# Optimization experiments

Measured on AMD Instinct MI355X. Metric: run time of the kernel, lower is better.

## Reference

```python
import jax, jax.numpy as jnp
import numpy as np

N, E = 50000, 800000
ND, ED, H, L = 128, 32, 128, 4


def _mlp2(x, w1, b1, w2, b2):
    return jax.nn.relu(x @ w1 + b1) @ w2 + b2


def _layer_norm(x, g, b, eps=1e-5):
    m = jnp.mean(x, axis=-1, keepdims=True)
    v = jnp.var(x, axis=-1, keepdims=True)
    return (x - m) * jax.lax.rsqrt(v + eps) * g + b


def setup_inputs() -> dict:
    key = jax.random.key(0)
    ks = iter(jax.random.split(key, 40))
    r = lambda *s: jax.random.normal(next(ks), s, jnp.float32) * 0.05
    return dict(
        x=r(N, ND),
        edge_attr=r(E, ED),
        h_prev=r(N, H),
        enc_w1=r(ND, H), enc_b1=jnp.zeros((H,), jnp.float32),
        enc_w2=r(H, H), enc_b2=jnp.zeros((H,), jnp.float32),
        et_w1=r(L, 2 * H + ED, H), et_b1=jnp.zeros((L, H), jnp.float32),
        et_w2=r(L, H, H), et_b2=jnp.zeros((L, H), jnp.float32),
        msg_w1=r(L, H, H), msg_b1=jnp.zeros((L, H), jnp.float32),
        msg_w2=r(L, H, H), msg_b2=jnp.zeros((L, H), jnp.float32),
        upd_w1=r(L, 2 * H, H), upd_b1=jnp.zeros((L, H), jnp.float32),
        upd_w2=r(L, H, H), upd_b2=jnp.zeros((L, H), jnp.float32),
        ln_g=jnp.ones((H,), jnp.float32), ln_b=jnp.zeros((H,), jnp.float32),
        gru_wih=r(3 * H, H), gru_whh=r(3 * H, H),
        gru_bih=jnp.zeros((3 * H,), jnp.float32),
        gru_bhh=jnp.zeros((3 * H,), jnp.float32),
        edge_index=jax.random.randint(next(ks), (2, E), 0, N, jnp.int32),
    )


def reference(x, edge_attr, h_prev,
              enc_w1, enc_b1, enc_w2, enc_b2,
              et_w1, et_b1, et_w2, et_b2,
              msg_w1, msg_b1, msg_w2, msg_b2,
              upd_w1, upd_b1, upd_w2, upd_b2,
              ln_g, ln_b,
              gru_wih, gru_whh, gru_bih, gru_bhh,
              edge_index):
    src, dst = edge_index[0], edge_index[1]  # PyG: x_j = x[src], x_i = x[dst]
    n_nodes = x.shape[0]
    h = _mlp2(x, enc_w1, enc_b1, enc_w2, enc_b2)  # [N, H]
    for l in range(et_w1.shape[0]):
        x_i = h[dst]                                  # [E, H] gather (target)
        x_j = h[src]                                  # [E, H] gather (source)
        e_in = jnp.concatenate([x_i, x_j, edge_attr], axis=-1)  # [E, 2H+ED]
        e_emb = _mlp2(e_in, et_w1[l], et_b1[l], et_w2[l], et_b2[l])
        msg = _mlp2(e_emb, msg_w1[l], msg_b1[l], msg_w2[l], msg_b2[l])
        aggr = jax.ops.segment_sum(msg, dst, num_segments=n_nodes)  # [N, H]
        h_new = _mlp2(jnp.concatenate([h, aggr], axis=-1),
                      upd_w1[l], upd_b1[l], upd_w2[l], upd_b2[l])
        h = _layer_norm(h + h_new, ln_g, ln_b)
    # GRUCell(input=h, hidden=h_prev), torch semantics
    gi = h @ gru_wih.T + gru_bih          # [N, 3H]
    gh = h_prev @ gru_whh.T + gru_bhh     # [N, 3H]
    i_r, i_z, i_n = jnp.split(gi, 3, axis=-1)
    h_r, h_z, h_n = jnp.split(gh, 3, axis=-1)
    r = jax.nn.sigmoid(i_r + h_r)
    z = jax.nn.sigmoid(i_z + h_z)
    n = jnp.tanh(i_n + r * h_n)
    return (1.0 - z) * n + z * h_prev
```

## Files before the change

### kernel.cpp

```cpp
#include <hip/hip_runtime.h>
#include <hip/hip_bf16.h>
#include <cstdint>

#define NN 50000
#define NE 800000

typedef _Float16 f16;
typedef f16 f16x8 __attribute__((ext_vector_type(8)));
typedef f16 f16x4 __attribute__((ext_vector_type(4)));
typedef float f32x4 __attribute__((ext_vector_type(4)));

#define TB_STR 136

__global__ void hist_kernel(const int* __restrict__ edst, int* __restrict__ deg) {
  int e = blockIdx.x * 256 + threadIdx.x;
  if (e < NE) atomicAdd(&deg[edst[e]], 1);
}

__global__ void scan_kernel(const int* __restrict__ deg, int* __restrict__ offs, int n) {
  __shared__ int tmp[256];
  __shared__ int carry;
  const int tid = threadIdx.x;
  if (tid == 0) carry = 0;
  __syncthreads();
  for (int base = 0; base < n; base += 1024) {
    int v[4]; int s = 0;
#pragma unroll
    for (int j = 0; j < 4; ++j) {
      int idx = base + tid * 4 + j;
      v[j] = (idx < n) ? deg[idx] : 0;
      s += v[j];
    }
    tmp[tid] = s;
    __syncthreads();
    for (int ofs = 1; ofs < 256; ofs <<= 1) {
      int t = (tid >= ofs) ? tmp[tid - ofs] : 0;
      __syncthreads();
      tmp[tid] += t;
      __syncthreads();
    }
    int excl = carry + tmp[tid] - s;
#pragma unroll
    for (int j = 0; j < 4; ++j) {
      int idx = base + tid * 4 + j;
      if (idx < n) offs[idx] = excl;
      excl += v[j];
    }
    __syncthreads();
    if (tid == 255) carry += tmp[255];
    __syncthreads();
  }
  if (tid == 0) offs[n] = carry;
}

__global__ void copy_cursor_kernel(const int* __restrict__ offs, int* __restrict__ cursor) {
  int i = blockIdx.x * 256 + threadIdx.x;
  if (i < NN) cursor[i] = offs[i];
}

__global__ void fill_kernel(const int* __restrict__ edst, int* __restrict__ cursor,
                            int* __restrict__ eord) {
  int e = blockIdx.x * 256 + threadIdx.x;
  if (e < NE) {
    int p = atomicAdd(&cursor[edst[e]], 1);
    eord[p] = e;
  }
}

__global__ void permute_kernel(const int* __restrict__ eord,
                               const int* __restrict__ esrc,
                               const int* __restrict__ edst,
                               const float* __restrict__ ea,
                               int* __restrict__ dstp, int* __restrict__ esp,
                               f16* __restrict__ ea16p) {
  int i = blockIdx.x * 256 + threadIdx.x;
  if (i >= NE) return;
  int e = eord[i];
  dstp[i] = edst[e];
  esp[i] = esrc[e];
  const float* sp = ea + (size_t)e * 32;
  f16* dp = ea16p + (size_t)i * 32;
#pragma unroll
  for (int j = 0; j < 4; ++j) {
    float4 u0 = *(const float4*)(sp + j * 8), u1 = *(const float4*)(sp + j * 8 + 4);
    f16x8 v = {(f16)u0.x, (f16)u0.y, (f16)u0.z, (f16)u0.w,
               (f16)u1.x, (f16)u1.y, (f16)u1.z, (f16)u1.w};
    *(f16x8*)(dp + j * 8) = v;
  }
}

__global__ void pack_w_kernel(const float* __restrict__ et_w1,
                              const float* __restrict__ et_w2,
                              const float* __restrict__ msg_w1,
                              const float* __restrict__ msg_w2,
                              f16* __restrict__ wpack) {
  int idx = blockIdx.x * 256 + threadIdx.x;
  if (idx >= 4 * 86016) return;
  int l = idx / 86016;
  int rem = idx - l * 86016;
  int unit = rem >> 9;
  int e = rem & 511;
  int ln = e >> 3, i = e & 7;
  const float* src;
  int ul;
  if (unit < 72)       { src = et_w1  + (size_t)l * 288 * 128; ul = unit; }
  else if (unit < 104) { src = et_w2  + (size_t)l * 128 * 128; ul = unit - 72; }
  else if (unit < 136) { src = msg_w1 + (size_t)l * 128 * 128; ul = unit - 104; }
  else                 { src = msg_w2 + (size_t)l * 128 * 128; ul = unit - 136; }
  int kc = ul >> 3, ct = ul & 7;
  int k = kc * 32 + (ln >> 4) * 8 + i;
  int col = ct * 16 + (ln & 15);
  wpack[idx] = (f16)src[k * 128 + col];
}

__global__ void pack_upd_kernel(const float* __restrict__ upd_w1,
                                const float* __restrict__ upd_w2,
                                f16* __restrict__ wpu) {
  int idx = blockIdx.x * 256 + threadIdx.x;
  if (idx >= 4 * 96 * 512) return;
  int l = idx / (96 * 512);
  int rem = idx - l * (96 * 512);
  int unit = rem >> 9, e = rem & 511, ln = e >> 3, i = e & 7;
  const float* src;
  int ul;
  if (unit < 64) { src = upd_w1 + (size_t)l * 256 * 128; ul = unit; }
  else           { src = upd_w2 + (size_t)l * 128 * 128; ul = unit - 64; }
  int kc = ul >> 3, ct = ul & 7;
  int k = kc * 32 + (ln >> 4) * 8 + i;
  int col = ct * 16 + (ln & 15);
  wpu[idx] = (f16)src[k * 128 + col];
}

__global__ void pack_gru_kernel(const float* __restrict__ wih,
                                const float* __restrict__ whh,
                                const float* __restrict__ bih,
                                const float* __restrict__ bhh,
                                f16* __restrict__ wg, float* __restrict__ brz) {
  int idx = blockIdx.x * 256 + threadIdx.x;
  if (idx < 256) brz[idx] = bih[idx] + bhh[idx];
  if (idx >= 192 * 512) return;
  int unit = idx >> 9, e = idx & 511, ln = e >> 3, i = e & 7;
  int krow = (ln >> 4) * 8 + i;
  int cl16 = ln & 15;
  f16 val;
  if (unit < 128) {
    int kc = unit >> 4, ctg = unit & 15;
    int k = kc * 32 + krow;
    int col = ctg * 16 + cl16;
    float w = (k < 128) ? wih[col * 128 + k] : whh[col * 128 + (k - 128)];
    val = (f16)w;
  } else if (unit < 160) {
    int ul = unit - 128;
    int k = (ul >> 3) * 32 + krow;
    int col = (ul & 7) * 16 + cl16;
    val = (f16)wih[(256 + col) * 128 + k];
  } else {
    int ul = unit - 160;
    int k = (ul >> 3) * 32 + krow;
    int col = (ul & 7) * 16 + cl16;
    val = (f16)whh[(256 + col) * 128 + k];
  }
  wg[idx] = val;
}

__global__ void pack_enc_kernel(const float* __restrict__ w1,
                                const float* __restrict__ w2,
                                f16* __restrict__ wpenc) {
  int idx = blockIdx.x * 256 + threadIdx.x;
  if (idx >= 64 * 512) return;
  int unit = idx >> 9, e = idx & 511, ln = e >> 3, i = e & 7;
  const float* src = (unit < 32) ? w1 : w2;
  int ul = unit & 31;
  int k = (ul >> 3) * 32 + (ln >> 4) * 8 + i;
  int col = (ul & 7) * 16 + (ln & 15);
  wpenc[idx] = (f16)src[k * 128 + col];
}

__global__ void cvt_x_kernel(const float* __restrict__ x, f16* __restrict__ x16) {
  int idx = blockIdx.x * 256 + threadIdx.x;
  if (idx >= NN * 16) return;
  const float* sp = x + (size_t)idx * 8;
  float4 u0 = *(const float4*)sp, u1 = *(const float4*)(sp + 4);
  f16x8 v = {(f16)u0.x, (f16)u0.y, (f16)u0.z, (f16)u0.w,
             (f16)u1.x, (f16)u1.y, (f16)u1.z, (f16)u1.w};
  *(f16x8*)(x16 + (size_t)idx * 8) = v;
}

#define EDGE_ACC_INIT(BIAS)                                                    \
  _Pragma("unroll") for (int ct = 0; ct < 4; ++ct) {                           \
    float bv_ = (BIAS)[wc * 64 + ct * 16 + cl];                                \
    acc[0][ct] = (f32x4){bv_, bv_, bv_, bv_};                                  \
    acc[1][ct] = acc[0][ct];                                                   \
  }

#define EDGE_MFMA_KC(A0, A1, UNIT)                                             \
  _Pragma("unroll") for (int ct = 0; ct < 4; ++ct) {                           \
    f16x8 b_ = *(const f16x8*)&wp[(size_t)(((UNIT) + wc * 4 + ct) * 64 + lane) * 8]; \
    acc[0][ct] = __builtin_amdgcn_mfma_f32_16x16x32_f16(A0, b_, acc[0][ct], 0, 0, 0); \
    acc[1][ct] = __builtin_amdgcn_mfma_f32_16x16x32_f16(A1, b_, acc[1][ct], 0, 0, 0); \
  }

#define EDGE_GEMM_LDS(APTR, UNIT0, BIAS)                                       \
  {                                                                            \
    EDGE_ACC_INIT(BIAS);                                                       \
    _Pragma("unroll") for (int kc = 0; kc < 4; ++kc) {                         \
      f16x8 a0_ = *(const f16x8*)&(APTR)[(wr * 32 + cl) * TB_STR + kc * 32 + kh * 8]; \
      f16x8 a1_ = *(const f16x8*)&(APTR)[(wr * 32 + 16 + cl) * TB_STR + kc * 32 + kh * 8]; \
      EDGE_MFMA_KC(a0_, a1_, (UNIT0) + kc * 8);                                \
    }                                                                          \
  }

#define EDGE_STORE(DST, RELU)                                                  \
  _Pragma("unroll") for (int rt = 0; rt < 2; ++rt)                             \
    _Pragma("unroll") for (int ct = 0; ct < 4; ++ct)                           \
      _Pragma("unroll") for (int i = 0; i < 4; ++i) {                          \
        float v_ = acc[rt][ct][i];                                             \
        if (RELU) v_ = fmaxf(v_, 0.f);                                         \
        (DST)[(wr * 32 + rt * 16 + kh * 4 + i) * TB_STR + wc * 64 + ct * 16 + cl] = (f16)v_; \
      }

__global__ __launch_bounds__(256, 6)
void edge_mfma_kernel(const f16* __restrict__ h16, const f16* __restrict__ ea16p,
                      const int* __restrict__ esp, const int* __restrict__ dstp,
                      const f16* __restrict__ wp,
                      const float* __restrict__ b1, const float* __restrict__ b2,
                      const float* __restrict__ b3, const float* __restrict__ b4,
                      float* __restrict__ aggrf) {
  __shared__ f16 buf[64 * TB_STR];
  __shared__ int eidx[128];
  const int tid = threadIdx.x;
  const int lane = tid & 63;
  const int wv = tid >> 6;
  const int wr = wv >> 1, wc = wv & 1;
  const int cl = lane & 15;
  const int kh = lane >> 4;
  const int e0 = blockIdx.x * 64;
  if (tid < 64) eidx[tid] = dstp[e0 + tid];
  else if (tid < 128) eidx[tid] = esp[e0 + tid - 64];
  __syncthreads();

  const int r0 = wr * 32 + cl, r1 = r0 + 16;
  const f16* pd0 = h16 + (size_t)eidx[r0] * 128 + kh * 8;
  const f16* pd1 = h16 + (size_t)eidx[r1] * 128 + kh * 8;
  const f16* ps0 = h16 + (size_t)eidx[64 + r0] * 128 + kh * 8;
  const f16* ps1 = h16 + (size_t)eidx[64 + r1] * 128 + kh * 8;
  const f16* pe0 = ea16p + (size_t)(e0 + r0) * 32 + kh * 8;
  const f16* pe1 = ea16p + (size_t)(e0 + r1) * 32 + kh * 8;

  f32x4 acc[2][4];
  EDGE_ACC_INIT(b1);
#pragma unroll
  for (int kc = 0; kc < 4; ++kc) {
    f16x8 a0_ = *(const f16x8*)(pd0 + kc * 32);
    f16x8 a1_ = *(const f16x8*)(pd1 + kc * 32);
    EDGE_MFMA_KC(a0_, a1_, kc * 8);
  }
#pragma unroll
  for (int kc = 4; kc < 8; ++kc) {
    f16x8 a0_ = *(const f16x8*)(ps0 + (kc - 4) * 32);
    f16x8 a1_ = *(const f16x8*)(ps1 + (kc - 4) * 32);
    EDGE_MFMA_KC(a0_, a1_, kc * 8);
  }
  {
    f16x8 a0_ = *(const f16x8*)pe0;
    f16x8 a1_ = *(const f16x8*)pe1;
    EDGE_MFMA_KC(a0_, a1_, 64);
  }
  EDGE_STORE(buf, 1);
  __syncthreads();
  EDGE_GEMM_LDS(buf, 72, b2);
  __syncthreads();
  EDGE_STORE(buf, 0);
  __syncthreads();
  EDGE_GEMM_LDS(buf, 104, b3);
  __syncthreads();
  EDGE_STORE(buf, 1);
  __syncthreads();
  EDGE_GEMM_LDS(buf, 136, b4);
  __syncthreads();
  EDGE_STORE(buf, 0);
  __syncthreads();
  {
    const int c = tid & 127;
    const int rbeg = (tid >> 7) * 32;
    float sum = 0.f;
    int cur = eidx[rbeg];
    bool openL = true;
    for (int r = rbeg; r < rbeg + 32; ++r) {
      sum += (float)buf[r * TB_STR + c];
      bool last = (r == rbeg + 31);
      int nxt = last ? -1 : eidx[r + 1];
      if (last || nxt != cur) {
        float* ap = aggrf + (size_t)cur * 128 + c;
        if (openL || last) unsafeAtomicAdd(ap, sum);
        else *ap = sum;
        sum = 0.f; cur = nxt; openL = false;
      }
    }
  }
}

__global__ __launch_bounds__(256, 4)
void encoder_mfma_kernel(const f16* __restrict__ x16, const f16* __restrict__ wp,
                         const float* __restrict__ b1, const float* __restrict__ b2,
                         f16* __restrict__ h16out) {
  __shared__ f16 buf[64 * TB_STR];
  const int tid = threadIdx.x;
  const int lane = tid & 63;
  const int wv = tid >> 6;
  const int wr = wv >> 1, wc = wv & 1;
  const int cl = lane & 15;
  const int kh = lane >> 4;
  const int r0 = blockIdx.x * 64;
  const int gr0 = min(r0 + wr * 32 + cl, NN - 1);
  const int gr1 = min(r0 + wr * 32 + 16 + cl, NN - 1);
  const f16* px0 = x16 + (size_t)gr0 * 128 + kh * 8;
  const f16* px1 = x16 + (size_t)gr1 * 128 + kh * 8;
  f32x4 acc[2][4];
  EDGE_ACC_INIT(b1);
#pragma unroll
  for (int kc = 0; kc < 4; ++kc) {
    f16x8 a0_ = *(const f16x8*)(px0 + kc * 32);
    f16x8 a1_ = *(const f16x8*)(px1 + kc * 32);
    EDGE_MFMA_KC(a0_, a1_, kc * 8);
  }
  EDGE_STORE(buf, 1);
  __syncthreads();
  EDGE_GEMM_LDS(buf, 32, b2);
  __syncthreads();
  EDGE_STORE(buf, 0);
  __syncthreads();
#pragma unroll
  for (int it = 0; it < 4; ++it) {
    int f = tid + it * 256;
    int row = f >> 4, c8 = f & 15;
    int grow = r0 + row;
    if (grow < NN) {
      f16x8 v = *(const f16x8*)&buf[row * TB_STR + c8 * 8];
      *(f16x8*)(h16out + (size_t)grow * 128 + c8 * 8) = v;
    }
  }
}

__global__ __launch_bounds__(256, 2)
void gru_mfma_kernel(const f16* __restrict__ h16, const float* __restrict__ hprev,
                     const f16* __restrict__ wg, const float* __restrict__ brz,
                     const float* __restrict__ bih, const float* __restrict__ bhh,
                     float* __restrict__ out) {
  __shared__ f16 ac[64 * 264];
  __shared__ f16 rz[64 * 264];
  const int tid = threadIdx.x;
  const int lane = tid & 63;
  const int wv = tid >> 6;
  const int wr = wv >> 1, wc = wv & 1;
  const int cl = lane & 15;
  const int kh = lane >> 4;
  const int r0 = blockIdx.x * 64;
#pragma unroll
  for (int it = 0; it < 8; ++it) {
    int f = tid + it * 256;
    int row = f >> 5, c8 = f & 31;
    int grow = r0 + row;
    f16x8 v = {};
    if (grow < NN) {
      if (c8 < 16) {
        v = *(const f16x8*)(h16 + (size_t)grow * 128 + c8 * 8);
      } else {
        const float* sp = hprev + (size_t)grow * 128 + (c8 - 16) * 8;
        float4 u0 = *(const float4*)sp, u1 = *(const float4*)(sp + 4);
        v = (f16x8){(f16)u0.x, (f16)u0.y, (f16)u0.z, (f16)u0.w,
                    (f16)u1.x, (f16)u1.y, (f16)u1.z, (f16)u1.w};
      }
    }
    *(f16x8*)&ac[row * 264 + c8 * 8] = v;
  }
  __syncthreads();
  {
    f32x4 az[4][4];
#pragma unroll
    for (int ct = 0; ct < 4; ++ct) {
      float bv = brz[wv * 64 + ct * 16 + cl];
#pragma unroll
      for (int rt = 0; rt < 4; ++rt) az[rt][ct] = (f32x4){bv, bv, bv, bv};
    }
#pragma unroll
    for (int kc = 0; kc < 8; ++kc) {
      f16x8 a_[4];
#pragma unroll
      for (int rt = 0; rt < 4; ++rt)
        a_[rt] = *(const f16x8*)&ac[(rt * 16 + cl) * 264 + kc * 32 + kh * 8];
#pragma unroll
      for (int ct = 0; ct < 4; ++ct) {
        f16x8 b_ = *(const f16x8*)&wg[(size_t)((kc * 16 + wv * 4 + ct) * 64 + lane) * 8];
#pragma unroll
        for (int rt = 0; rt < 4; ++rt)
          az[rt][ct] = __builtin_amdgcn_mfma_f32_16x16x32_f16(a_[rt], b_, az[rt][ct], 0, 0, 0);
      }
    }
#pragma unroll
    for (int rt = 0; rt < 4; ++rt)
#pragma unroll
      for (int ct = 0; ct < 4; ++ct)
#pragma unroll
        for (int i = 0; i < 4; ++i) {
          float sg = 1.f / (1.f + __expf(-az[rt][ct][i]));
          rz[(rt * 16 + kh * 4 + i) * 264 + wv * 64 + ct * 16 + cl] = (f16)sg;
        }
  }
  __syncthreads();
  f32x4 ai_[2][4], ah_[2][4];
#pragma unroll
  for (int ct = 0; ct < 4; ++ct) {
    float bi = bih[256 + wc * 64 + ct * 16 + cl];
    float bh = bhh[256 + wc * 64 + ct * 16 + cl];
    ai_[0][ct] = (f32x4){bi, bi, bi, bi}; ai_[1][ct] = ai_[0][ct];
    ah_[0][ct] = (f32x4){bh, bh, bh, bh}; ah_[1][ct] = ah_[0][ct];
  }
#pragma unroll
  for (int kc = 0; kc < 4; ++kc) {
    f16x8 a0 = *(const f16x8*)&ac[(wr * 32 + cl) * 264 + kc * 32 + kh * 8];
    f16x8 a1 = *(const f16x8*)&ac[(wr * 32 + 16 + cl) * 264 + kc * 32 + kh * 8];
    f16x8 p0 = *(const f16x8*)&ac[(wr * 32 + cl) * 264 + 128 + kc * 32 + kh * 8];
    f16x8 p1 = *(const f16x8*)&ac[(wr * 32 + 16 + cl) * 264 + 128 + kc * 32 + kh * 8];
#pragma unroll
    for (int ct = 0; ct < 4; ++ct) {
      f16x8 bi_ = *(const f16x8*)&wg[(size_t)(((128 + kc * 8 + wc * 4 + ct)) * 64 + lane) * 8];
      f16x8 bh_ = *(const f16x8*)&wg[(size_t)(((160 + kc * 8 + wc * 4 + ct)) * 64 + lane) * 8];
      ai_[0][ct] = __builtin_amdgcn_mfma_f32_16x16x32_f16(a0, bi_, ai_[0][ct], 0, 0, 0);
      ai_[1][ct] = __builtin_amdgcn_mfma_f32_16x16x32_f16(a1, bi_, ai_[1][ct], 0, 0, 0);
      ah_[0][ct] = __builtin_amdgcn_mfma_f32_16x16x32_f16(p0, bh_, ah_[0][ct], 0, 0, 0);
      ah_[1][ct] = __builtin_amdgcn_mfma_f32_16x16x32_f16(p1, bh_, ah_[1][ct], 0, 0, 0);
    }
  }
#pragma unroll
  for (int rt = 0; rt < 2; ++rt)
#pragma unroll
    for (int ct = 0; ct < 4; ++ct)
#pragma unroll
      for (int i = 0; i < 4; ++i) {
        int row = wr * 32 + rt * 16 + kh * 4 + i;
        int col = wc * 64 + ct * 16 + cl;
        int grow = r0 + row;
        if (grow < NN) {
          float r_ = (float)rz[row * 264 + col];
          float z_ = (float)rz[row * 264 + 128 + col];
          float n_ = tanhf(ai_[rt][ct][i] + r_ * ah_[rt][ct][i]);
          float hpv = (float)ac[row * 264 + 128 + col];
          out[(size_t)grow * 128 + col] = (1.f - z_) * n_ + z_ * hpv;
        }
      }
}

#define MFMA_T(APTR, ASTR, ASWZ, NKC, UNIT0, BIAS)                             \
  {                                                                            \
    _Pragma("unroll") for (int nt = 0; nt < 2; ++nt) {                         \
      f32x4 bv_ = *(const f32x4*)((BIAS) + wv * 32 + nt * 16 + kh * 4);        \
      _Pragma("unroll") for (int et = 0; et < 4; ++et) acc[nt][et] = bv_;      \
    }                                                                          \
    _Pragma("unroll 2") for (int kc = 0; kc < (NKC); ++kc) {                   \
      f16x8 wfr_[2];                                                           \
      _Pragma("unroll") for (int nt = 0; nt < 2; ++nt)                         \
        wfr_[nt] = *(const f16x8*)&wp[(size_t)(((UNIT0) + kc * 8 + wv * 2 + nt) * 64 + lane) * 8]; \
      _Pragma("unroll") for (int et = 0; et < 4; ++et) {                       \
        int r_ = et * 16 + cl;                                                 \
        int idx_ = r_ * (ASTR) + kc * 32 + kh * 8;                             \
        if (ASWZ) idx_ ^= ((r_ & 7) << 3);                                     \
        f16x8 efr_ = *(const f16x8*)&(APTR)[idx_];                             \
        _Pragma("unroll") for (int nt = 0; nt < 2; ++nt)                       \
          acc[nt][et] = __builtin_amdgcn_mfma_f32_16x16x32_f16(wfr_[nt], efr_, acc[nt][et], 0, 0, 0); \
      }                                                                        \
    }                                                                          \
  }

#define STORE_T(DPTR, RELU)                                                    \
  _Pragma("unroll") for (int nt = 0; nt < 2; ++nt)                             \
    _Pragma("unroll") for (int et = 0; et < 4; ++et) {                         \
      float v0_ = acc[nt][et][0], v1_ = acc[nt][et][1],                        \
            v2_ = acc[nt][et][2], v3_ = acc[nt][et][3];                        \
      if (RELU) { v0_ = fmaxf(v0_, 0.f); v1_ = fmaxf(v1_, 0.f);                \
                  v2_ = fmaxf(v2_, 0.f); v3_ = fmaxf(v3_, 0.f); }              \
      int r_ = et * 16 + cl;                                                   \
      int idx_ = (r_ * 128 + wv * 32 + nt * 16 + kh * 4) ^ ((r_ & 7) << 3);    \
      *(f16x4*)&(DPTR)[idx_] = (f16x4){(f16)v0_, (f16)v1_, (f16)v2_, (f16)v3_};\
    }

__global__ __launch_bounds__(256, 2)
void update_mfma_kernel(const f16* __restrict__ h16, const float* __restrict__ aggr,
                        const f16* __restrict__ wp,
                        const float* __restrict__ b1, const float* __restrict__ b2,
                        const float* __restrict__ lng, const float* __restrict__ lnb,
                        f16* __restrict__ h16out) {
  __shared__ f16 ua[64 * 264];
  __shared__ f16 tb[64 * 128];
  __shared__ f16 emb[64 * 128];
  const int tid = threadIdx.x;
  const int lane = tid & 63;
  const int wv = tid >> 6;
  const int cl = lane & 15;
  const int kh = lane >> 4;
  const int r0 = blockIdx.x * 64;
#pragma unroll
  for (int it = 0; it < 8; ++it) {
    int f = tid + it * 256;
    int row = f >> 5, c8 = f & 31;
    int grow = r0 + row;
    f16x8 v = {};
    if (grow < NN) {
      if (c8 < 16) {
        v = *(const f16x8*)(h16 + (size_t)grow * 128 + c8 * 8);
      } else {
        const float* sp = aggr + (size_t)grow * 128 + (c8 - 16) * 8;
        float4 u0 = *(const float4*)sp, u1 = *(const float4*)(sp + 4);
        v = (f16x8){(f16)u0.x, (f16)u0.y, (f16)u0.z, (f16)u0.w,
                    (f16)u1.x, (f16)u1.y, (f16)u1.z, (f16)u1.w};
      }
    }
    *(f16x8*)&ua[row * 264 + c8 * 8] = v;
  }
  __syncthreads();
  f32x4 acc[2][4];
  MFMA_T(ua, 264, 0, 8, 0, b1);
  STORE_T(tb, 1);
  __syncthreads();
  MFMA_T(tb, 128, 1, 4, 64, b2);
  STORE_T(emb, 0);
  __syncthreads();
  {
    const int row = tid >> 2, q = tid & 3;
    const int grow = r0 + row;
    float y[32];
    float s = 0.f, ss = 0.f;
#pragma unroll
    for (int j = 0; j < 4; ++j) {
      int col = q * 32 + j * 8;
      int ei = (row * 128 + col) ^ ((row & 7) << 3);
      f16x8 ev = *(const f16x8*)&emb[ei];
      f16x8 rv = *(const f16x8*)&ua[row * 264 + col];
#pragma unroll
      for (int e = 0; e < 8; ++e) {
        float t = (float)ev[e] + (float)rv[e];
        y[j * 8 + e] = t; s += t; ss += t * t;
      }
    }
    s += __shfl_xor(s, 1);  s += __shfl_xor(s, 2);
    ss += __shfl_xor(ss, 1); ss += __shfl_xor(ss, 2);
    float mean = s * (1.f / 128.f);
    float var = ss * (1.f / 128.f) - mean * mean;
    float rstd = rsqrtf(var + 1e-5f);
    if (grow < NN) {
#pragma unroll
      for (int j = 0; j < 4; ++j) {
        int col = q * 32 + j * 8;
        const float4 g0 = *(const float4*)(lng + col), g1 = *(const float4*)(lng + col + 4);
        const float4 q0 = *(const float4*)(lnb + col), q1 = *(const float4*)(lnb + col + 4);
        float gv[8] = {g0.x, g0.y, g0.z, g0.w, g1.x, g1.y, g1.z, g1.w};
        float bv[8] = {q0.x, q0.y, q0.z, q0.w, q1.x, q1.y, q1.z, q1.w};
        f16x8 o;
#pragma unroll
        for (int e = 0; e < 8; ++e)
          o[e] = (f16)((y[j * 8 + e] - mean) * rstd * gv[e] + bv[e]);
        *(f16x8*)(h16out + (size_t)grow * 128 + col) = o;
      }
    }
  }
}

extern "C" void kernel_launch(void* const* d_in, const int* in_sizes, int n_in,
                              void* d_out, int out_size, void* d_ws, size_t ws_size,
                              hipStream_t stream) {
  (void)in_sizes; (void)n_in; (void)out_size; (void)ws_size;
  const float* x         = (const float*)d_in[0];
  const float* edge_attr = (const float*)d_in[1];
  const float* h_prev    = (const float*)d_in[2];
  const float* enc_w1    = (const float*)d_in[3];
  const float* enc_b1    = (const float*)d_in[4];
  const float* enc_w2    = (const float*)d_in[5];
  const float* enc_b2    = (const float*)d_in[6];
  const float* et_w1     = (const float*)d_in[7];
  const float* et_b1     = (const float*)d_in[8];
  const float* et_w2     = (const float*)d_in[9];
  const float* et_b2     = (const float*)d_in[10];
  const float* msg_w1    = (const float*)d_in[11];
  const float* msg_b1    = (const float*)d_in[12];
  const float* msg_w2    = (const float*)d_in[13];
  const float* msg_b2    = (const float*)d_in[14];
  const float* upd_w1    = (const float*)d_in[15];
  const float* upd_b1    = (const float*)d_in[16];
  const float* upd_w2    = (const float*)d_in[17];
  const float* upd_b2    = (const float*)d_in[18];
  const float* ln_g      = (const float*)d_in[19];
  const float* ln_b      = (const float*)d_in[20];
  const float* gru_wih   = (const float*)d_in[21];
  const float* gru_whh   = (const float*)d_in[22];
  const float* gru_bih   = (const float*)d_in[23];
  const float* gru_bhh   = (const float*)d_in[24];
  const int* edge_index  = (const int*)d_in[25];
  const int* esrc = edge_index;
  const int* edst = edge_index + NE;

  float* ws    = (float*)d_ws;
  float* aggrf = ws;
  float* wreg  = ws + (size_t)NN * 128;
  f16*   wg    = (f16*)wreg;
  float* brz   = wreg + 49152;
  f16*   wpenc = (f16*)(brz + 256);
  f16*   h16a  = (f16*)(wreg + 98304);
  f16*   h16b  = h16a + (size_t)NN * 128;
  f16*   wpe   = h16b + (size_t)NN * 128;
  f16*   wpu   = wpe + 4 * 86016;
  f16*   ea16p = wpu + 4 * 96 * 512;

  int* iout   = (int*)d_out;
  int* deg    = iout;
  int* offs   = iout + 51200;
  int* cursor = iout + 102400;
  int* eord   = iout + 153600;
  int* dstp   = iout + 153600 + NE;
  int* esp    = iout + 153600 + 2 * NE;
  f16* x16    = (f16*)(iout + 2600000);

  hipMemsetAsync(deg, 0, NN * sizeof(int), stream);
  hist_kernel<<<(NE + 255) / 256, 256, 0, stream>>>(edst, deg);
  scan_kernel<<<1, 256, 0, stream>>>(deg, offs, NN);
  copy_cursor_kernel<<<(NN + 255) / 256, 256, 0, stream>>>(offs, cursor);
  fill_kernel<<<(NE + 255) / 256, 256, 0, stream>>>(edst, cursor, eord);
  permute_kernel<<<(NE + 255) / 256, 256, 0, stream>>>(eord, esrc, edst, edge_attr,
                                                       dstp, esp, ea16p);

  pack_w_kernel<<<(4 * 86016 + 255) / 256, 256, 0, stream>>>(et_w1, et_w2, msg_w1, msg_w2, wpe);
  pack_upd_kernel<<<(4 * 96 * 512 + 255) / 256, 256, 0, stream>>>(upd_w1, upd_w2, wpu);
  pack_gru_kernel<<<(192 * 512 + 255) / 256, 256, 0, stream>>>(gru_wih, gru_whh,
                                                               gru_bih, gru_bhh, wg, brz);
  pack_enc_kernel<<<(64 * 512 + 255) / 256, 256, 0, stream>>>(enc_w1, enc_w2, wpenc);
  cvt_x_kernel<<<(NN * 16 + 255) / 256, 256, 0, stream>>>(x, x16);
  encoder_mfma_kernel<<<(NN + 63) / 64, 256, 0, stream>>>(x16, wpenc, enc_b1, enc_b2, h16a);

  f16* hc = h16a;
  f16* hn = h16b;
  for (int l = 0; l < 4; ++l) {
    hipMemsetAsync(aggrf, 0, (size_t)NN * 128 * sizeof(float), stream);
    edge_mfma_kernel<<<NE / 64, 256, 0, stream>>>(
        hc, ea16p, esp, dstp,
        wpe + (size_t)l * 86016,
        et_b1 + l * 128, et_b2 + l * 128,
        msg_b1 + l * 128, msg_b2 + l * 128,
        aggrf);
    update_mfma_kernel<<<(NN + 63) / 64, 256, 0, stream>>>(
        hc, aggrf,
        wpu + (size_t)l * 96 * 512,
        upd_b1 + l * 128, upd_b2 + l * 128,
        ln_g, ln_b, hn);
    f16* t = hc; hc = hn; hn = t;
  }
  gru_mfma_kernel<<<(NN + 63) / 64, 256, 0, stream>>>(hc, h_prev, wg, brz,
                                                      gru_bih, gru_bhh, (float*)d_out);
}
```

Measured before the change: 1.259 ms.

## Fold edge-MLP second linear and message first linear into one matrix

Because e_emb = relu(...)@W2+b2 has no activation before msg_w1, the two linears are precomputed as W23 = W2@W3 and b23 = b2@W3 + b3 by a small kernel. The edge kernel then runs three 128x128 GEMMs per edge tile instead of four and drops one LDS store/sync round trip. This removes a quarter of the per-edge MLP compute. It changes fp16 rounding, since the intermediate e_emb is no longer materialized, and it adds a tiny setup kernel plus workspace for the fp32 folded weights.

Measured after the change: 1.168 ms, median of 2. 7.3% less time.

```diff
diff --git a/kernel.cpp b/kernel.cpp
--- a/kernel.cpp
+++ b/kernel.cpp
@@ -89,24 +89,62 @@
   }
 }
 
+__global__ void w23_kernel(const float* __restrict__ et_w2,
+                           const float* __restrict__ et_b2,
+                           const float* __restrict__ msg_w1,
+                           const float* __restrict__ msg_b1,
+                           float* __restrict__ w23, float* __restrict__ b23) {
+  const int l = blockIdx.x >> 3, cc = blockIdx.x & 7;
+  const float* W2 = et_w2 + (size_t)l * 16384;
+  const float* W3 = msg_w1 + (size_t)l * 16384;
+  __shared__ float w3s[128][17];
+  const int tid = threadIdx.x;
+#pragma unroll
+  for (int it = 0; it < 8; ++it) {
+    int f = tid + it * 256;
+    int m = f >> 4, n = f & 15;
+    w3s[m][n] = W3[m * 128 + cc * 16 + n];
+  }
+  __syncthreads();
+  const int k = tid >> 1, nh = (tid & 1) * 8;
+  float s[8] = {};
+  for (int m = 0; m < 128; ++m) {
+    float w2v = W2[k * 128 + m];
+#pragma unroll
+    for (int j = 0; j < 8; ++j) s[j] = fmaf(w2v, w3s[m][nh + j], s[j]);
+  }
+#pragma unroll
+  for (int j = 0; j < 8; ++j)
+    w23[(size_t)l * 16384 + k * 128 + cc * 16 + nh + j] = s[j];
+  if (k == 0) {
+    float sb[8] = {};
+    for (int m = 0; m < 128; ++m) {
+      float b2v = et_b2[l * 128 + m];
+#pragma unroll
+      for (int j = 0; j < 8; ++j) sb[j] = fmaf(b2v, w3s[m][nh + j], sb[j]);
+    }
+#pragma unroll
+    for (int j = 0; j < 8; ++j)
+      b23[l * 128 + cc * 16 + nh + j] = sb[j] + msg_b1[l * 128 + cc * 16 + nh + j];
+  }
+}
+
 __global__ void pack_w_kernel(const float* __restrict__ et_w1,
-                              const float* __restrict__ et_w2,
-                              const float* __restrict__ msg_w1,
+                              const float* __restrict__ w23,
                               const float* __restrict__ msg_w2,
                               f16* __restrict__ wpack) {
   int idx = blockIdx.x * 256 + threadIdx.x;
-  if (idx >= 4 * 86016) return;
-  int l = idx / 86016;
-  int rem = idx - l * 86016;
+  if (idx >= 4 * 69632) return;
+  int l = idx / 69632;
+  int rem = idx - l * 69632;
   int unit = rem >> 9;
   int e = rem & 511;
   int ln = e >> 3, i = e & 7;
   const float* src;
   int ul;
   if (unit < 72)       { src = et_w1  + (size_t)l * 288 * 128; ul = unit; }
-  else if (unit < 104) { src = et_w2  + (size_t)l * 128 * 128; ul = unit - 72; }
-  else if (unit < 136) { src = msg_w1 + (size_t)l * 128 * 128; ul = unit - 104; }
-  else                 { src = msg_w2 + (size_t)l * 128 * 128; ul = unit - 136; }
+  else if (unit < 104) { src = w23    + (size_t)l * 16384;     ul = unit - 72; }
+  else                 { src = msg_w2 + (size_t)l * 16384;     ul = unit - 104; }
   int kc = ul >> 3, ct = ul & 7;
   int k = kc * 32 + (ln >> 4) * 8 + i;
   int col = ct * 16 + (ln & 15);
@@ -223,8 +261,8 @@
 void edge_mfma_kernel(const f16* __restrict__ h16, const f16* __restrict__ ea16p,
                       const int* __restrict__ esp, const int* __restrict__ dstp,
                       const f16* __restrict__ wp,
-                      const float* __restrict__ b1, const float* __restrict__ b2,
-                      const float* __restrict__ b3, const float* __restrict__ b4,
+                      const float* __restrict__ b1, const float* __restrict__ b23,
+                      const float* __restrict__ b4,
                       float* __restrict__ aggrf) {
   __shared__ f16 buf[64 * TB_STR];
   __shared__ int eidx[128];
@@ -268,15 +306,11 @@
   }
   EDGE_STORE(buf, 1);
   __syncthreads();
-  EDGE_GEMM_LDS(buf, 72, b2);
-  __syncthreads();
-  EDGE_STORE(buf, 0);
-  __syncthreads();
-  EDGE_GEMM_LDS(buf, 104, b3);
+  EDGE_GEMM_LDS(buf, 72, b23);
   __syncthreads();
   EDGE_STORE(buf, 1);
   __syncthreads();
-  EDGE_GEMM_LDS(buf, 136, b4);
+  EDGE_GEMM_LDS(buf, 104, b4);
   __syncthreads();
   EDGE_STORE(buf, 0);
   __syncthreads();
@@ -607,8 +641,10 @@
   f16*   h16a  = (f16*)(wreg + 98304);
   f16*   h16b  = h16a + (size_t)NN * 128;
   f16*   wpe   = h16b + (size_t)NN * 128;
-  f16*   wpu   = wpe + 4 * 86016;
+  f16*   wpu   = wpe + 4 * 69632;
   f16*   ea16p = wpu + 4 * 96 * 512;
+  float* w23f  = (float*)(ea16p + (size_t)NE * 32);
+  float* b23f  = w23f + 4 * 16384;
 
   int* iout   = (int*)d_out;
   int* deg    = iout;
@@ -627,7 +663,8 @@
   permute_kernel<<<(NE + 255) / 256, 256, 0, stream>>>(eord, esrc, edst, edge_attr,
                                                        dstp, esp, ea16p);
 
-  pack_w_kernel<<<(4 * 86016 + 255) / 256, 256, 0, stream>>>(et_w1, et_w2, msg_w1, msg_w2, wpe);
+  w23_kernel<<<32, 256, 0, stream>>>(et_w2, et_b2, msg_w1, msg_b1, w23f, b23f);
+  pack_w_kernel<<<(4 * 69632 + 255) / 256, 256, 0, stream>>>(et_w1, w23f, msg_w2, wpe);
   pack_upd_kernel<<<(4 * 96 * 512 + 255) / 256, 256, 0, stream>>>(upd_w1, upd_w2, wpu);
   pack_gru_kernel<<<(192 * 512 + 255) / 256, 256, 0, stream>>>(gru_wih, gru_whh,
                                                                gru_bih, gru_bhh, wg, brz);
@@ -641,9 +678,8 @@
     hipMemsetAsync(aggrf, 0, (size_t)NN * 128 * sizeof(float), stream);
     edge_mfma_kernel<<<NE / 64, 256, 0, stream>>>(
         hc, ea16p, esp, dstp,
-        wpe + (size_t)l * 86016,
-        et_b1 + l * 128, et_b2 + l * 128,
-        msg_b1 + l * 128, msg_b2 + l * 128,
+        wpe + (size_t)l * 69632,
+        et_b1 + l * 128, b23f + l * 128, msg_b2 + l * 128,
         aggrf);
     update_mfma_kernel<<<(NN + 63) / 64, 256, 0, stream>>>(
         hc, aggrf,
```
